# Performance work log

Measured on AMD Instinct MI355X. Metric: run time of the kernel, lower is better.

Reference implementation:

```python
import jax, jax.numpy as jnp
import numpy as np

B, C, H, W = 4, 64, 128, 128
HID = 256
Q = H * W


def setup_inputs() -> dict:
    key = jax.random.key(0)
    ks = jax.random.split(key, 8)
    inp = jax.random.normal(ks[0], (B, C, H, W), jnp.float32)
    coord = jax.random.uniform(ks[1], (B, Q, 2), jnp.float32, -1.0, 1.0)
    # cell ~ 2/H (size of a high-res pixel in normalized coords), slightly jittered
    cell = (2.0 / H) * (1.0 + 0.1 * jax.random.uniform(ks[2], (B, Q, 2), jnp.float32))
    sc = 1.0 / np.sqrt(C * 9)
    coef_w = jax.random.normal(ks[3], (HID, C, 3, 3), jnp.float32) * sc
    coef_b = jax.random.normal(ks[4], (HID,), jnp.float32) * 0.01
    freq_w = jax.random.normal(ks[5], (HID, C, 3, 3), jnp.float32) * sc
    freq_b = jax.random.normal(ks[6], (HID,), jnp.float32) * 0.01
    phase_w = jax.random.normal(ks[7], (HID // 2, 2), jnp.float32) * 0.5
    return dict(inp=inp, coord=coord, cell=cell, coef_w=coef_w, coef_b=coef_b,
                freq_w=freq_w, freq_b=freq_b, phase_w=phase_w)


def _conv3(x, w, b):
    # 3x3 conv, stride 1, pad 1, NCHW
    y = jax.lax.conv_general_dilated(x, w, (1, 1), ((1, 1), (1, 1)),
                                     dimension_numbers=('NCHW', 'OIHW', 'NCHW'))
    return y + b[None, :, None, None]


def reference(inp, coord, cell, coef_w, coef_b, freq_w, freq_b, phase_w):
    bs, q = coord.shape[0], coord.shape[1]
    h, w = inp.shape[2], inp.shape[3]
    coef = _conv3(inp, coef_w, coef_b)           # (B,HID,H,W)
    freq = _conv3(inp, freq_w, freq_b)           # (B,HID,H,W)
    coef_f = coef.reshape(bs, -1, h * w)
    freq_f = freq.reshape(bs, -1, h * w)
    rx = 1.0 / h                                 # 2/h/2
    ry = 1.0 / w
    eps_shift = 1e-6
    hw = jnp.array([h, w], jnp.float32)
    rel_cell = cell * hw                         # (B,Q,2)
    phase = rel_cell @ phase_w.T                 # (B,Q,HID//2)
    outputs, areas = [], []
    last_raw_area = None
    for vx in (-1.0, 1.0):
        for vy in (-1.0, 1.0):
            c = coord + jnp.array([vx * rx + eps_shift, vy * ry + eps_shift], jnp.float32)
            c = jnp.clip(c, -1.0 + 1e-6, 1.0 - 1e-6)
            # nearest grid_sample, align_corners=False (round-half-even like nearbyint)
            iy = jnp.round(((c[..., 0] + 1.0) * h - 1.0) * 0.5)
            ix = jnp.round(((c[..., 1] + 1.0) * w - 1.0) * 0.5)
            iy = jax.lax.stop_gradient(jnp.clip(iy, 0, h - 1).astype(jnp.int32))
            ix = jax.lax.stop_gradient(jnp.clip(ix, 0, w - 1).astype(jnp.int32))
            idx = iy * w + ix                    # (B,Q)
            q_coef = jnp.take_along_axis(coef_f, idx[:, None, :], axis=2).transpose(0, 2, 1)  # (B,Q,HID)
            q_freq = jnp.take_along_axis(freq_f, idx[:, None, :], axis=2).transpose(0, 2, 1)
            # make_coord value at the gathered pixel
            q_coord = jnp.stack([-1.0 + (2.0 * iy.astype(jnp.float32) + 1.0) / h,
                                 -1.0 + (2.0 * ix.astype(jnp.float32) + 1.0) / w], axis=-1)
            rel = (coord - q_coord) * hw         # (B,Q,2)
            # split q_freq into consecutive pairs, stack -> (B,Q,2,HID//2)
            f = q_freq.reshape(bs, q, -1, 2).swapaxes(-1, -2)
            f = jnp.sum(f * rel[..., None], axis=-2) + phase     # (B,Q,HID//2)
            f = jnp.concatenate([jnp.cos(jnp.pi * f), jnp.sin(jnp.pi * f)], axis=-1)  # (B,Q,HID)
            out = (q_coef * f).reshape(bs, h, w, -1).transpose(0, 3, 1, 2)  # (B,HID,H,W)
            last_raw_area = jnp.abs(rel[..., 0] * rel[..., 1])
            outputs.append(out)
            areas.append(last_raw_area + 1e-9)
    tot_area = areas[0] + areas[1] + areas[2] + areas[3]
    # Faithful to the source: a SINGLE weight from the last corner's raw area
    # is applied to every corner output (the per-corner area swap is unused).
    weight = (last_raw_area / tot_area).reshape(bs, h, w, 1).transpose(0, 3, 1, 2)
    ret = (outputs[0] + outputs[1] + outputs[2] + outputs[3]) * weight
    return ret
```

## Files before the change

kernel.cpp:

```cpp
#include <hip/hip_runtime.h>

typedef unsigned short u16;
typedef _Float16 f16;

#define CIN   64
#define HH    128
#define WW    128
#define NPIX  16384
#define HID   256
#define MTOT  512
#define KTOT  576
#define NB    4
#define WELEM 294912
#define XROW  130
#define XROWS 16900
#define RECB  768

#define SHM  ((float)(-0.0078125 + 1e-6))
#define SHP  ((float)( 0.0078125 + 1e-6))
#define CLO  ((float)(-1.0 + 1e-6))
#define CHI  ((float)( 1.0 - 1e-6))
#define PIF  3.14159265358979323846f

#define QSCL   1024.0f
#define QISCL  (1.0f / 1024.0f)
#define Q8SCL  16.0f
#define Q8ISCL 0.0625f

using f32x4 = __attribute__((ext_vector_type(4))) float;
using f16x8 = __attribute__((ext_vector_type(8))) _Float16;

typedef __attribute__((address_space(1))) const void gas_void;
typedef __attribute__((address_space(3))) void las_void;
__device__ __forceinline__ void gload16(const void* g, void* l) {
  __builtin_amdgcn_global_load_lds((gas_void*)g, (las_void*)l, 16, 0, 0);
}

__device__ __forceinline__ unsigned packq(float a, float b) {
  float fa = fminf(fmaxf(a * QSCL, -32767.f), 32767.f);
  float fb = fminf(fmaxf(b * QSCL, -32767.f), 32767.f);
  int ia = (int)rintf(fa), ib = (int)rintf(fb);
  return ((unsigned)(unsigned short)(short)ia) | (((unsigned)(unsigned short)(short)ib) << 16);
}
__device__ __forceinline__ unsigned pack8(float a, float b, float c, float d) {
  int ia = (int)rintf(fminf(fmaxf(a * Q8SCL, -127.f), 127.f));
  int ib = (int)rintf(fminf(fmaxf(b * Q8SCL, -127.f), 127.f));
  int ic = (int)rintf(fminf(fmaxf(c * Q8SCL, -127.f), 127.f));
  int id = (int)rintf(fminf(fmaxf(d * Q8SCL, -127.f), 127.f));
  return (ia & 255) | ((ib & 255) << 8) | ((ic & 255) << 16) | ((id & 255) << 24);
}

__global__ __launch_bounds__(256) void lte_prep_w(
    const float* __restrict__ cw, const float* __restrict__ fw,
    f16* __restrict__ Awp) {
  int id = blockIdx.x * 256 + threadIdx.x;
  if (id >= WELEM) return;
  int e  = id & 7;
  int l  = (id >> 3) & 63;
  int mi = (id >> 9) & 3;
  int r  = id >> 11;
  int ks = r & 1;
  int r2 = r >> 1;
  int s  = r2 % 9;
  int q  = r2 / 9;
  int wr = q & 1;
  int mt = q >> 1;
  int m  = mt * 128 + wr * 64 + mi * 16 + (l & 15);
  int ch = (ks * 4 + (l >> 4)) * 8 + e;
  const float* src = (m < HID) ? cw : fw;
  Awp[id] = (f16)src[(m & 255) * KTOT + ch * 9 + s];
}

__global__ __launch_bounds__(256) void lte_prep_x(
    const float* __restrict__ inp, f16* __restrict__ xp) {
  int id = blockIdx.x * 256 + threadIdx.x;
  if (id >= NB * XROWS) return;
  int b  = id / XROWS;
  int rr = id - b * XROWS;
  int yy = rr / XROW;
  int pc = rr - yy * XROW;
  int x  = pc - 1;
  int y  = yy - 1;
  f16* op = xp + (size_t)id * 64;
  if ((unsigned)y < 128u && (unsigned)x < 128u) {
    const float* ip = inp + (size_t)b * CIN * NPIX + y * WW + x;
    const int p7 = pc & 7;
#pragma unroll
    for (int q = 0; q < 8; ++q) {
      f16x8 v;
#pragma unroll
      for (int k = 0; k < 8; ++k) v[k] = (f16)ip[(((q ^ p7) << 3) + k) * NPIX];
      *(f16x8*)(op + q * 8) = v;
    }
  } else {
    f16x8 z = {};
#pragma unroll
    for (int q = 0; q < 8; ++q) *(f16x8*)(op + q * 8) = z;
  }
}

__global__ __launch_bounds__(256, 3) void lte_conv_gemm(
    const f16* __restrict__ xp, const f16* __restrict__ Awp,
    const float* __restrict__ coef_b, const float* __restrict__ freq_b,
    char* __restrict__ YT) {
  __shared__ f16 Bs[3 * 136 * 64];

  const int t  = threadIdx.x;
  const int bx = blockIdx.x;
  const int mt = blockIdx.y;
  const int bb = blockIdx.z;
  const int l  = t & 63;
  const int w  = t >> 6;
  const int wr = __builtin_amdgcn_readfirstlane(w >> 1);
  const int wc = __builtin_amdgcn_readfirstlane(w & 1);
  const int lm = l & 15;

  f32x4 acc[4][4] = {};

  const f16* xb = xp + (size_t)bb * XROWS * 64;
  const f16* Aw = Awp + (size_t)((mt * 2 + wr) * 9) * 4096 + l * 8;

  for (int c = w; c < 51; c += 4) {
    const int rr = c / 17, cc = c - rr * 17;
    gload16(xb + (size_t)((bx + rr) * XROW + cc * 8) * 64 + l * 8,
            Bs + (rr * 136 + cc * 8) * 64);
  }

  f16x8 afb[2][4];
#define LOAD_AF(buf_, h_)                                                    \
  {                                                                          \
    const f16* ap_ = Aw + ((h_) >> 1) * 4096 + ((h_) & 1) * 2048;            \
    afb[buf_][0] = *(const f16x8*)(ap_);                                     \
    afb[buf_][1] = *(const f16x8*)(ap_ + 512);                               \
    afb[buf_][2] = *(const f16x8*)(ap_ + 1024);                              \
    afb[buf_][3] = *(const f16x8*)(ap_ + 1536);                              \
  }

  LOAD_AF(0, 0)
  asm volatile("s_waitcnt vmcnt(0)" ::: "memory");
  __builtin_amdgcn_s_barrier();

#pragma unroll
  for (int h = 0; h < 18; ++h) {
    const int s  = h >> 1;
    const int ks = h & 1;
    if (h < 17) LOAD_AF((h + 1) & 1, h + 1)
    const int ky = s / 3, kx = s - 3 * (s / 3);
    const int jl = ks * 4 + (l >> 4);
    f16x8 bg[4];
#pragma unroll
    for (int ni = 0; ni < 4; ++ni) {
      const int xc = wc * 64 + ni * 16 + lm + kx;
      bg[ni] = *(const f16x8*)&Bs[(ky * 136 + xc) * 64 + ((jl ^ (xc & 7)) << 3)];
    }
#pragma unroll
    for (int mi = 0; mi < 4; ++mi)
#pragma unroll
      for (int ni = 0; ni < 4; ++ni)
        acc[mi][ni] = __builtin_amdgcn_mfma_f32_16x16x32_f16(afb[h & 1][mi], bg[ni], acc[mi][ni], 0, 0, 0);
  }

  __syncthreads();
  const float* bias = (mt < 2) ? (coef_b + mt * 128) : (freq_b + (mt - 2) * 128);
  const int rj = (l >> 4) * 4;
  if (mt < 2) {
    char* lt8 = (char*)Bs;
#pragma unroll
    for (int mi = 0; mi < 4; ++mi) {
      const int bm = wr * 64 + mi * 16 + rj;
      const float b0 = bias[bm], b1 = bias[bm + 1], b2 = bias[bm + 2], b3 = bias[bm + 3];
#pragma unroll
      for (int ni = 0; ni < 4; ++ni) {
        const int p = wc * 64 + ni * 16 + lm;
        f32x4 v = acc[mi][ni];
        *(unsigned*)&lt8[p * 144 + bm] = pack8(v[0] + b0, v[1] + b1, v[2] + b2, v[3] + b3);
      }
    }
    __syncthreads();
    char* yb8 = YT + (size_t)(bb * NPIX + bx * 128) * RECB + mt * 128;
#pragma unroll
    for (int it = 0; it < 4; ++it) {
      const int p = it * 32 + (t >> 3);
      const int off = (t & 7) * 16;
      uint4 v = *(const uint4*)&lt8[p * 144 + off];
      *(uint4*)&yb8[(size_t)p * RECB + off] = v;
    }
  } else {
    short* lt = (short*)Bs;
#pragma unroll
    for (int mi = 0; mi < 4; ++mi) {
      const int bm = wr * 64 + mi * 16 + rj;
      const float b0 = bias[bm], b1 = bias[bm + 1], b2 = bias[bm + 2], b3 = bias[bm + 3];
#pragma unroll
      for (int ni = 0; ni < 4; ++ni) {
        const int p = wc * 64 + ni * 16 + lm;
        f32x4 v = acc[mi][ni];
        uint2 q2; q2.x = packq(v[0] + b0, v[1] + b1); q2.y = packq(v[2] + b2, v[3] + b3);
        *(uint2*)&lt[p * 138 + bm] = q2;
      }
    }
    __syncthreads();
    short* yb = (short*)(YT + (size_t)(bb * NPIX + bx * 128) * RECB + 256) + (mt - 2) * 128;
    const int lp = l >> 5;
    const int c4 = (l & 31) * 4;
#pragma unroll
    for (int it = 0; it < 16; ++it) {
      const int p = it * 8 + w * 2 + lp;
      uint2 v = *(const uint2*)&lt[p * 138 + c4];
      *(uint2*)&yb[(size_t)p * (RECB / 2) + c4] = v;
    }
  }
}

__global__ __launch_bounds__(128) void lte_sample(
    const char* __restrict__ YT, const float* __restrict__ coord,
    const float* __restrict__ cell, const float* __restrict__ phase_w,
    float* __restrict__ out) {
  __shared__ float lout[256 * 17];
  const int j     = threadIdx.x;
  const int q0    = blockIdx.x * 16;
  const int b     = q0 >> 14;
  const int q0loc = q0 & (NPIX - 1);
  const float pw0 = phase_w[2 * j], pw1 = phase_w[2 * j + 1];
  const char* Yb = YT + (size_t)b * NPIX * RECB;

  for (int qi = 0; qi < 16; ++qi) {
    const int qg = q0 + qi;
    const float c0  = coord[2 * qg], c1 = coord[2 * qg + 1];
    const float ce0 = cell[2 * qg],  ce1 = cell[2 * qg + 1];
    const float ph  = (ce0 * 128.0f) * pw0 + (ce1 * 128.0f) * pw1;
    float accC = 0.f, accS = 0.f, tot = 0.f, a3 = 0.f;
#pragma unroll
    for (int ci = 0; ci < 4; ++ci) {
      const float s0 = (ci & 2) ? SHP : SHM;
      const float s1 = (ci & 1) ? SHP : SHM;
      float cx = fminf(fmaxf(c0 + s0, CLO), CHI);
      float cy = fminf(fmaxf(c1 + s1, CLO), CHI);
      float ty = ((cx + 1.0f) * 128.0f - 1.0f) * 0.5f;
      float tx = ((cy + 1.0f) * 128.0f - 1.0f) * 0.5f;
      float fy = fminf(fmaxf(rintf(ty), 0.f), 127.f);
      float fx = fminf(fmaxf(rintf(tx), 0.f), 127.f);
      int iy = (int)fy, ix = (int)fx;
      float qcy = -1.0f + (2.0f * fy + 1.0f) * (1.0f / 128.0f);
      float qcx = -1.0f + (2.0f * fx + 1.0f) * (1.0f / 128.0f);
      float rel0 = (c0 - qcy) * 128.0f;
      float rel1 = (c1 - qcx) * 128.0f;
      float ar = fabsf(rel0 * rel1);
      tot += ar + 1e-9f;
      if (ci == 3) a3 = ar;
      const char* bp = Yb + (size_t)(iy * 128 + ix) * RECB;
      float coefA = (float)(*(const signed char*)(bp + j)) * Q8ISCL;
      float coefB = (float)(*(const signed char*)(bp + 128 + j)) * Q8ISCL;
      int u = *(const int*)(bp + 256 + 4 * j);
      float f0 = (float)((short)(u & 0xFFFF)) * QISCL;
      float f1 = (float)((short)(u >> 16)) * QISCL;
      float f = f0 * rel0 + f1 * rel1 + ph;
      float ang = PIF * f;
      accC += coefA * __cosf(ang);
      accS += coefB * __sinf(ang);
    }
    const float wgt = a3 / tot;
    lout[j * 17 + qi]         = accC * wgt;
    lout[(j + 128) * 17 + qi] = accS * wgt;
  }
  __syncthreads();
#pragma unroll
  for (int pass = 0; pass < 8; ++pass) {
    int c  = pass * 32 + (j >> 2);
    int qf = (j & 3) * 4;
    float4 v;
    v.x = lout[c * 17 + qf];     v.y = lout[c * 17 + qf + 1];
    v.z = lout[c * 17 + qf + 2]; v.w = lout[c * 17 + qf + 3];
    *(float4*)(out + (((size_t)(b * 256 + c)) << 14) + q0loc + qf) = v;
  }
}

extern "C" void kernel_launch(void* const* d_in, const int* in_sizes, int n_in,
                              void* d_out, int out_size, void* d_ws, size_t ws_size,
                              hipStream_t stream) {
  const float* inp     = (const float*)d_in[0];
  const float* coord   = (const float*)d_in[1];
  const float* cell    = (const float*)d_in[2];
  const float* coef_w  = (const float*)d_in[3];
  const float* coef_b  = (const float*)d_in[4];
  const float* freq_w  = (const float*)d_in[5];
  const float* freq_b  = (const float*)d_in[6];
  const float* phase_w = (const float*)d_in[7];
  float* out = (float*)d_out;

  f16* Awp = (f16*)d_ws;
  f16* xp  = (f16*)((char*)d_ws + (size_t)WELEM * 2);
  char* YT = (char*)d_ws + (size_t)WELEM * 2 + ((size_t)NB * XROWS + 8) * 64 * 2;

  lte_prep_w<<<dim3(1152), dim3(256), 0, stream>>>(coef_w, freq_w, Awp);
  lte_prep_x<<<dim3((NB * XROWS + 255) / 256), dim3(256), 0, stream>>>(inp, xp);
  lte_conv_gemm<<<dim3(128, 4, 4), dim3(256), 0, stream>>>(xp, Awp, coef_b, freq_b, YT);
  lte_sample<<<dim3(4096), dim3(128), 0, stream>>>(YT, coord, cell, phase_w, out);
}
```

Baseline: 121.5 us.

## Double-buffer sampled feature records into LDS via async global_load_lds

The sample kernel now computes corner indices for groups of four queries ahead of time and stages the 768-byte feature records into a double-buffered LDS area using global_load_lds. The loads for the next group are issued while the current group is consumed. The aim is to hide the latency of the dependent gather loads that previously stalled each query iteration. In exchange it adds about 24KB of LDS per block plus extra barriers, which may reduce occupancy, and it relies on manual waitcnt handling.

```diff
diff --git a/kernel.cpp b/kernel.cpp
--- a/kernel.cpp
+++ b/kernel.cpp
@@ -34,6 +34,9 @@
 typedef __attribute__((address_space(3))) void las_void;
 __device__ __forceinline__ void gload16(const void* g, void* l) {
   __builtin_amdgcn_global_load_lds((gas_void*)g, (las_void*)l, 16, 0, 0);
+}
+__device__ __forceinline__ void gload4(const void* g, void* l) {
+  __builtin_amdgcn_global_load_lds((gas_void*)g, (las_void*)l, 4, 0, 0);
 }
 
 __device__ __forceinline__ unsigned packq(float a, float b) {
@@ -217,51 +220,101 @@
     const float* __restrict__ cell, const float* __restrict__ phase_w,
     float* __restrict__ out) {
   __shared__ float lout[256 * 17];
+  __shared__ char  rbuf[2][16 * RECB];
   const int j     = threadIdx.x;
+  const int wv    = j >> 6;
+  const int l     = j & 63;
   const int q0    = blockIdx.x * 16;
   const int b     = q0 >> 14;
   const int q0loc = q0 & (NPIX - 1);
   const float pw0 = phase_w[2 * j], pw1 = phase_w[2 * j + 1];
   const char* Yb = YT + (size_t)b * NPIX * RECB;
 
-  for (int qi = 0; qi < 16; ++qi) {
-    const int qg = q0 + qi;
-    const float c0  = coord[2 * qg], c1 = coord[2 * qg + 1];
-    const float ce0 = cell[2 * qg],  ce1 = cell[2 * qg + 1];
-    const float ph  = (ce0 * 128.0f) * pw0 + (ce1 * 128.0f) * pw1;
-    float accC = 0.f, accS = 0.f, tot = 0.f, a3 = 0.f;
-#pragma unroll
-    for (int ci = 0; ci < 4; ++ci) {
-      const float s0 = (ci & 2) ? SHP : SHM;
-      const float s1 = (ci & 1) ? SHP : SHM;
-      float cx = fminf(fmaxf(c0 + s0, CLO), CHI);
-      float cy = fminf(fmaxf(c1 + s1, CLO), CHI);
-      float ty = ((cx + 1.0f) * 128.0f - 1.0f) * 0.5f;
-      float tx = ((cy + 1.0f) * 128.0f - 1.0f) * 0.5f;
-      float fy = fminf(fmaxf(rintf(ty), 0.f), 127.f);
-      float fx = fminf(fmaxf(rintf(tx), 0.f), 127.f);
-      int iy = (int)fy, ix = (int)fx;
-      float qcy = -1.0f + (2.0f * fy + 1.0f) * (1.0f / 128.0f);
-      float qcx = -1.0f + (2.0f * fx + 1.0f) * (1.0f / 128.0f);
-      float rel0 = (c0 - qcy) * 128.0f;
-      float rel1 = (c1 - qcx) * 128.0f;
-      float ar = fabsf(rel0 * rel1);
-      tot += ar + 1e-9f;
-      if (ci == 3) a3 = ar;
-      const char* bp = Yb + (size_t)(iy * 128 + ix) * RECB;
-      float coefA = (float)(*(const signed char*)(bp + j)) * Q8ISCL;
-      float coefB = (float)(*(const signed char*)(bp + 128 + j)) * Q8ISCL;
-      int u = *(const int*)(bp + 256 + 4 * j);
-      float f0 = (float)((short)(u & 0xFFFF)) * QISCL;
-      float f1 = (float)((short)(u >> 16)) * QISCL;
-      float f = f0 * rel0 + f1 * rel1 + ph;
-      float ang = PIF * f;
-      accC += coefA * __cosf(ang);
-      accS += coefB * __sinf(ang);
-    }
-    const float wgt = a3 / tot;
-    lout[j * 17 + qi]         = accC * wgt;
-    lout[(j + 128) * 17 + qi] = accS * wgt;
+  float ph[2][4], tot[2][4], a3[2][4];
+  float rel0[2][4][4], rel1[2][4][4];
+  int   off[2][4][4];
+
+#define PHASE_A(qn_)                                                         \
+  {                                                                          \
+    const int S_ = (qn_) & 1;                                                \
+    _Pragma("unroll")                                                        \
+    for (int qi = 0; qi < 4; ++qi) {                                         \
+      const int qg = q0 + (qn_) * 4 + qi;                                    \
+      const float c0 = coord[2 * qg], c1 = coord[2 * qg + 1];                \
+      const float ce0 = cell[2 * qg], ce1 = cell[2 * qg + 1];                \
+      ph[S_][qi] = (ce0 * 128.0f) * pw0 + (ce1 * 128.0f) * pw1;              \
+      tot[S_][qi] = 0.f;                                                     \
+      _Pragma("unroll")                                                      \
+      for (int ci = 0; ci < 4; ++ci) {                                       \
+        const float s0 = (ci & 2) ? SHP : SHM;                               \
+        const float s1 = (ci & 1) ? SHP : SHM;                               \
+        float cx = fminf(fmaxf(c0 + s0, CLO), CHI);                          \
+        float cy = fminf(fmaxf(c1 + s1, CLO), CHI);                          \
+        float ty = ((cx + 1.0f) * 128.0f - 1.0f) * 0.5f;                     \
+        float tx = ((cy + 1.0f) * 128.0f - 1.0f) * 0.5f;                     \
+        float fy = fminf(fmaxf(rintf(ty), 0.f), 127.f);                      \
+        float fx = fminf(fmaxf(rintf(tx), 0.f), 127.f);                      \
+        int iy = (int)fy, ix = (int)fx;                                      \
+        float qcy = -1.0f + (2.0f * fy + 1.0f) * (1.0f / 128.0f);            \
+        float qcx = -1.0f + (2.0f * fx + 1.0f) * (1.0f / 128.0f);            \
+        rel0[S_][qi][ci] = (c0 - qcy) * 128.0f;                              \
+        rel1[S_][qi][ci] = (c1 - qcx) * 128.0f;                              \
+        float ar = fabsf(rel0[S_][qi][ci] * rel1[S_][qi][ci]);               \
+        tot[S_][qi] += ar + 1e-9f;                                           \
+        if (ci == 3) a3[S_][qi] = ar;                                        \
+        off[S_][qi][ci] = (iy * 128 + ix) * RECB;                            \
+      }                                                                      \
+    }                                                                        \
+  }
+
+#define STAGE_Q(qn_)                                                         \
+  {                                                                          \
+    const int S_ = (qn_) & 1;                                                \
+    _Pragma("unroll")                                                        \
+    for (int i = 0; i < 8; ++i) {                                            \
+      const int r_ = wv * 8 + i;                                             \
+      const char* gb_ = Yb + off[S_][r_ >> 2][r_ & 3];                       \
+      char* lb_ = rbuf[S_] + r_ * RECB;                                      \
+      gload4(gb_ + l * 4,       lb_);                                        \
+      gload4(gb_ + 256 + l * 4, lb_ + 256);                                  \
+      gload4(gb_ + 512 + l * 4, lb_ + 512);                                  \
+    }                                                                        \
+  }
+
+  PHASE_A(0)
+  STAGE_Q(0)
+
+#pragma unroll
+  for (int qq = 0; qq < 4; ++qq) {
+    const int S = qq & 1;
+    if (qq < 3) PHASE_A(qq + 1)
+    asm volatile("s_waitcnt vmcnt(0)" ::: "memory");
+    __builtin_amdgcn_s_barrier();
+    __builtin_amdgcn_sched_barrier(0);
+    if (qq < 3) STAGE_Q(qq + 1)
+#pragma unroll
+    for (int qi = 0; qi < 4; ++qi) {
+      float accC = 0.f, accS = 0.f;
+#pragma unroll
+      for (int ci = 0; ci < 4; ++ci) {
+        const char* rp = rbuf[S] + (qi * 4 + ci) * RECB;
+        float coefA = (float)(*(const signed char*)(rp + j)) * Q8ISCL;
+        float coefB = (float)(*(const signed char*)(rp + 128 + j)) * Q8ISCL;
+        int u = *(const int*)(rp + 256 + 4 * j);
+        float f0 = (float)((short)(u & 0xFFFF)) * QISCL;
+        float f1 = (float)((short)(u >> 16)) * QISCL;
+        float f = f0 * rel0[S][qi][ci] + f1 * rel1[S][qi][ci] + ph[S][qi];
+        float ang = PIF * f;
+        accC += coefA * __cosf(ang);
+        accS += coefB * __sinf(ang);
+      }
+      const float wgt = a3[S][qi] / tot[S][qi];
+      lout[j * 17 + qq * 4 + qi]         = accC * wgt;
+      lout[(j + 128) * 17 + qq * 4 + qi] = accS * wgt;
+    }
+    asm volatile("s_waitcnt lgkmcnt(0)" ::: "memory");
+    __builtin_amdgcn_s_barrier();
+    __builtin_amdgcn_sched_barrier(0);
   }
   __syncthreads();
 #pragma unroll
```

Measured after the change: 214.2 us. +76.3%, slower.
